# Performance work log

Hardware: AMD Instinct MI355X
Metric: run time of the kernel (lower is better)

## Reference

```python
import jax, jax.numpy as jnp
import numpy as np

N, L, S, D = 8, 1024, 4096, 512
EPS = 1e-5

def layernorm(x, g, b):
    mu = jnp.mean(x, axis=-1, keepdims=True)
    var = jnp.var(x, axis=-1, keepdims=True)
    return (x - mu) * jax.lax.rsqrt(var + EPS) * g + b

def setup_inputs() -> dict:
    key = jax.random.key(0)
    ks = jax.random.split(key, 8)
    w = lambda k, shp: jax.random.normal(k, shp, dtype=jnp.float32) * 0.02
    return {
        "x": jax.random.normal(ks[0], (N, L, D), dtype=jnp.float32),
        "source": jax.random.normal(ks[1], (N, S, D), dtype=jnp.float32),
        "Wq": w(ks[2], (D, D)),
        "Wk": w(ks[3], (D, D)),
        "Wv": w(ks[4], (D, D)),
        "Wm": w(ks[5], (D, D)),
        "W1": w(ks[6], (2 * D, 2 * D)),
        "W2": w(ks[7], (2 * D, D)),
        "g1": jnp.ones((D,), jnp.float32),
        "b1": jnp.zeros((D,), jnp.float32),
        "g2": jnp.ones((D,), jnp.float32),
        "b2": jnp.zeros((D,), jnp.float32),
    }

def reference(x, source, Wq, Wk, Wv, Wm, W1, W2, g1, b1, g2, b2):
    # projections
    q = x @ Wq          # [N, L, D]
    k = source @ Wk     # [N, S, D]
    v = source @ Wv     # [N, S, D]
    # pairwise L2 distance via ||q||^2 + ||k||^2 - 2 q.k (avoids [N,L,S,D] tensor)
    q2 = jnp.sum(q * q, axis=-1)                      # [N, L]
    k2 = jnp.sum(k * k, axis=-1)                      # [N, S]
    qk = jnp.einsum('nlc,nsc->nls', q, k)             # [N, L, S]
    dist = jnp.sqrt(jnp.maximum(q2[:, :, None] + k2[:, None, :] - 2.0 * qk, 0.0))
    attn = jax.nn.softmax(dist, axis=2)               # softmax over S (note: +distance, as in source)
    message = jnp.einsum('nls,nsc->nlc', attn, v)     # [N, L, D]
    message = layernorm(message @ Wm, g1, b1)
    h = jnp.concatenate([x, message], axis=2)         # [N, L, 2D]
    message = jax.nn.relu(h @ W1) @ W2                # [N, L, D]
    message = layernorm(message, g2, b2)
    return x + message
```

## Files before the change

kernel.cpp:

```cpp
#include <hip/hip_runtime.h>
#include <stdint.h>

typedef unsigned short u16;
typedef __attribute__((ext_vector_type(8))) short bf16x8;
typedef __attribute__((ext_vector_type(4))) float f32x4;
typedef __attribute__((ext_vector_type(4))) unsigned int u32x4;

__device__ __forceinline__ u16 f2b(float f) {
  uint32_t u = __float_as_uint(f);
  u += 0x7fffu + ((u >> 16) & 1u);
  return (u16)(u >> 16);
}
__device__ __forceinline__ float b2f(u16 h) {
  return __uint_as_float(((uint32_t)h) << 16);
}
__device__ __forceinline__ uint32_t pack2bf(float a, float b) {
#if __has_builtin(__builtin_amdgcn_cvt_pk_bf16_f32)
  typedef __attribute__((ext_vector_type(2))) __bf16 bf16x2_t;
  bf16x2_t r = __builtin_amdgcn_cvt_pk_bf16_f32(a, b);
  return __builtin_bit_cast(uint32_t, r);
#else
  return (uint32_t)f2b(a) | ((uint32_t)f2b(b) << 16);
#endif
}
__device__ __forceinline__ float fast_sqrtf(float x) {
#if __has_builtin(__builtin_amdgcn_sqrtf)
  return __builtin_amdgcn_sqrtf(x);
#else
  return sqrtf(x);
#endif
}

__device__ __forceinline__ void gload_lds16(const u16* g, u16* l) {
  __builtin_amdgcn_global_load_lds(
      (const __attribute__((address_space(1))) void*)g,
      (__attribute__((address_space(3))) void*)l, 16, 0, 0);
}

enum { EPI_BF16_T = 0, EPI_BF16_T_SQ = 1, EPI_F32_T = 2, EPI_RELU_BF16_T = 3,
       EPI_EXP_T = 4 };

template <int EPI, bool BYFAST = false>
__device__ __forceinline__ void gemm_body(
    u16* smem, const u16* A, size_t sA, int lda,
    const u16* B, size_t sB, int ldb,
    void* C, size_t sC, int ldc, int K, size_t pStride,
    const float* e_col2, const float* e_row2, float* e_l,
    int lin, int gx, int gy) {
  u16* As = smem;
  u16* Bs = smem + 8192;
  const int t = threadIdx.x;
  const int batch = lin & 7;
  const int rest = lin >> 3;
  int bx, by, part;
  if (BYFAST) {
    by = rest % gy;
    const int rx = rest / gy;
    bx = rx % gx;
    part = rx / gx;
  } else {
    bx = rest % gx;
    const int ry = rest / gx;
    by = ry % gy;
    part = ry / gy;
  }
  const int m0 = by * 128, n0 = bx * 128;
  const int koff = part * K;
  const u16* Ab = A + (size_t)batch * sA + (size_t)m0 * lda + koff;
  const u16* Bb = B + (size_t)batch * sB + (size_t)n0 * ldb + koff;
  const int srow = t >> 3;
  const int skey = (srow & 3) | (((srow >> 3) & 1) << 2);
  const int scol = ((t & 7) ^ skey) << 3;
  const u16* aS = Ab + (size_t)srow * lda + scol;
  const u16* bS = Bb + (size_t)srow * ldb + scol;
  const size_t a32 = (size_t)32 * lda, b32 = (size_t)32 * ldb;
  u16* asDst = As + t * 8;
  u16* bsDst = Bs + t * 8;

  const int w = t >> 6, lane = t & 63;
  const int wm = (w >> 1) << 6, wn = (w & 1) << 6;
  const int qd = lane >> 4, l16 = lane & 15;
  const int rbase = ((l16 >> 2) << 3) + (l16 & 3);
  const int keyA = (l16 & 3) | (((l16 >> 2) & 1) << 2);
  const int keyB = (l16 & 3) | (((l16 >> 3) & 1) << 2);
  const u16* aRow0 = As + (wm + rbase) * 64;
  const u16* bRow0 = Bs + (wn + l16) * 64;

  f32x4 acc[4][4];
#pragma unroll
  for (int i = 0; i < 4; i++)
#pragma unroll
    for (int j = 0; j < 4; j++) acc[i][j] = (f32x4)0.0f;

  for (int k0 = 0; k0 < K; k0 += 64) {
    gload_lds16(aS, asDst);
    gload_lds16(aS + a32, asDst + 2048);
    gload_lds16(aS + 2 * a32, asDst + 4096);
    gload_lds16(aS + 3 * a32, asDst + 6144);
    gload_lds16(bS, bsDst);
    gload_lds16(bS + b32, bsDst + 2048);
    gload_lds16(bS + 2 * b32, bsDst + 4096);
    gload_lds16(bS + 3 * b32, bsDst + 6144);
    aS += 64;
    bS += 64;
    __syncthreads();
#pragma unroll
    for (int s = 0; s < 2; s++) {
      const int ca = (((qd | (s << 2)) ^ keyA) << 3);
      const int cb = (((qd | (s << 2)) ^ keyB) << 3);
      bf16x8 af[4], bfr[4];
      af[0] = *(const bf16x8*)(aRow0 + ca);
      af[1] = *(const bf16x8*)(aRow0 + 4 * 64 + ca);
      af[2] = *(const bf16x8*)(aRow0 + 32 * 64 + ca);
      af[3] = *(const bf16x8*)(aRow0 + 36 * 64 + ca);
#pragma unroll
      for (int i = 0; i < 4; i++)
        bfr[i] = *(const bf16x8*)(bRow0 + i * 16 * 64 + cb);
#pragma unroll
      for (int mi = 0; mi < 4; mi++)
#pragma unroll
        for (int ni = 0; ni < 4; ni++)
          acc[mi][ni] = __builtin_amdgcn_mfma_f32_16x16x32_bf16(
              af[mi], bfr[ni], acc[mi][ni], 0, 0, 0);
    }
    __syncthreads();
  }

  const size_t cbase = (size_t)part * pStride + (size_t)batch * sC;
  const int ncols = (int)(sC / ldc);

  if constexpr (EPI == EPI_EXP_T) {
    const int nrows = (int)(sA / lda);
    const float* col2 = e_col2 + (size_t)batch * ncols;
    const float* row2 = e_row2 + (size_t)batch * nrows;
    float* lb = e_l + (size_t)batch * ncols;
    float c2v[4];
#pragma unroll
    for (int ni = 0; ni < 4; ni++) c2v[ni] = col2[n0 + wn + ni * 16 + l16];
    float cs[4] = {0.f, 0.f, 0.f, 0.f};
#pragma unroll
    for (int p = 0; p < 2; p++) {
      const int prow = m0 + wm + p * 32 + qd * 8;
      float r2v[8];
#pragma unroll
      for (int r8 = 0; r8 < 8; r8++) r2v[r8] = row2[prow + r8];
#pragma unroll
      for (int ni = 0; ni < 4; ni++) {
        const int col = n0 + wn + ni * 16 + l16;
        float pv[8];
#pragma unroll
        for (int r = 0; r < 4; r++) {
          pv[r] = __expf(fast_sqrtf(
              fmaxf(c2v[ni] + r2v[r] - 2.0f * acc[2 * p][ni][r], 0.0f)));
          pv[4 + r] = __expf(fast_sqrtf(
              fmaxf(c2v[ni] + r2v[4 + r] - 2.0f * acc[2 * p + 1][ni][r], 0.0f)));
        }
#pragma unroll
        for (int j = 0; j < 8; j++) cs[ni] += pv[j];
        u32x4 wv;
        wv[0] = pack2bf(pv[0], pv[1]);
        wv[1] = pack2bf(pv[2], pv[3]);
        wv[2] = pack2bf(pv[4], pv[5]);
        wv[3] = pack2bf(pv[6], pv[7]);
        *(u32x4*)((u16*)C + cbase + (size_t)col * ldc + prow) = wv;
      }
    }
#pragma unroll
    for (int ni = 0; ni < 4; ni++) {
      cs[ni] += __shfl_xor(cs[ni], 16);
      cs[ni] += __shfl_xor(cs[ni], 32);
    }
    if (qd == 0) {
#pragma unroll
      for (int ni = 0; ni < 4; ni++)
        atomicAdd(lb + n0 + wn + ni * 16 + l16, cs[ni]);
    }
  } else if constexpr (EPI == EPI_F32_T) {
#pragma unroll
    for (int p = 0; p < 2; p++) {
      const int prow = m0 + wm + p * 32 + qd * 8;
#pragma unroll
      for (int ni = 0; ni < 4; ni++) {
        const int col = n0 + wn + ni * 16 + l16;
        float* dst = (float*)C + cbase + (size_t)col * ldc + prow;
        *(f32x4*)dst = acc[2 * p][ni];
        *(f32x4*)(dst + 4) = acc[2 * p + 1][ni];
      }
    }
  } else {
    float cs[4] = {0.f, 0.f, 0.f, 0.f};
#pragma unroll
    for (int p = 0; p < 2; p++) {
      const int prow = m0 + wm + p * 32 + qd * 8;
#pragma unroll
      for (int ni = 0; ni < 4; ni++) {
        const int col = n0 + wn + ni * 16 + l16;
        float v[8];
#pragma unroll
        for (int r = 0; r < 4; r++) {
          v[r] = acc[2 * p][ni][r];
          v[4 + r] = acc[2 * p + 1][ni][r];
        }
        if (EPI == EPI_RELU_BF16_T) {
#pragma unroll
          for (int j = 0; j < 8; j++) v[j] = fmaxf(v[j], 0.0f);
        }
        if (EPI == EPI_BF16_T_SQ) {
#pragma unroll
          for (int j = 0; j < 8; j++) cs[ni] += v[j] * v[j];
        }
        u32x4 wv;
        wv[0] = pack2bf(v[0], v[1]);
        wv[1] = pack2bf(v[2], v[3]);
        wv[2] = pack2bf(v[4], v[5]);
        wv[3] = pack2bf(v[6], v[7]);
        *(u32x4*)((u16*)C + cbase + (size_t)col * ldc + prow) = wv;
      }
    }
    if (EPI == EPI_BF16_T_SQ) {
#pragma unroll
      for (int ni = 0; ni < 4; ni++) {
        cs[ni] += __shfl_xor(cs[ni], 16);
        cs[ni] += __shfl_xor(cs[ni], 32);
      }
      if (qd == 0) {
#pragma unroll
        for (int ni = 0; ni < 4; ni++)
          atomicAdd(e_l + (size_t)batch * ncols + n0 + wn + ni * 16 + l16,
                    cs[ni]);
      }
    }
  }
}

template <int EPI>
__global__ __launch_bounds__(256, 2) void gemm_nt(
    const u16* __restrict__ A, size_t sA, int lda,
    const u16* __restrict__ B, size_t sB, int ldb,
    void* __restrict__ C, size_t sC, int ldc, int K, size_t pStride,
    const float* __restrict__ e_col2, const float* __restrict__ e_row2,
    float* __restrict__ e_l) {
  __shared__ __align__(16) u16 smem[16384];
  const int lin = blockIdx.x + gridDim.x * (blockIdx.y + gridDim.y * blockIdx.z);
  gemm_body<EPI>(smem, A, sA, lda, B, sB, ldb, C, sC, ldc, K, pStride,
                 e_col2, e_row2, e_l, lin, gridDim.x, gridDim.y);
}

__global__ __launch_bounds__(256, 2) void proj_fused(
    const u16* __restrict__ WqT, const u16* __restrict__ WkT,
    const u16* __restrict__ WvT, const u16* __restrict__ h,
    const u16* __restrict__ sb, u16* __restrict__ q, u16* __restrict__ kb,
    u16* __restrict__ vT, float* __restrict__ q2, float* __restrict__ k2) {
  __shared__ __align__(16) u16 smem[16384];
  const int lin = blockIdx.x;
  if (lin < 256) {
    gemm_body<EPI_BF16_T_SQ, true>(smem, WqT, 0, 512, h, (size_t)1024 * 1024,
                                   1024, q, (size_t)1024 * 512, 512, 512, 0,
                                   nullptr, nullptr, q2, lin, 8, 4);
  } else if (lin < 1280) {
    gemm_body<EPI_BF16_T_SQ, true>(smem, WkT, 0, 512, sb, (size_t)4096 * 512,
                                   512, kb, (size_t)4096 * 512, 512, 512, 0,
                                   nullptr, nullptr, k2, lin - 256, 32, 4);
  } else {
    gemm_body<EPI_BF16_T>(smem, sb, (size_t)4096 * 512, 512, WvT, 0, 512,
                          vT, (size_t)512 * 4096, 4096, 512, 0, nullptr,
                          nullptr, nullptr, lin - 1280, 4, 32);
  }
}

__global__ __launch_bounds__(256) void prep_all(
    const float* __restrict__ x, const float* __restrict__ sc,
    u16* __restrict__ h, u16* __restrict__ sb, float* __restrict__ q2,
    float* __restrict__ k2, float* __restrict__ lsum,
    const float* __restrict__ Wq, const float* __restrict__ Wk,
    const float* __restrict__ Wv, const float* __restrict__ Wm,
    const float* __restrict__ W1, const float* __restrict__ W2,
    u16* __restrict__ WqT, u16* __restrict__ WkT, u16* __restrict__ WvT,
    u16* __restrict__ WmT2, u16* __restrict__ W1T, u16* __restrict__ W2T) {
  __shared__ float tile[32][33];
  const int blk = blockIdx.x;
  if (blk < 20528) {
    const size_t i = (size_t)blk * 256 + threadIdx.x;
    if (i < 1048576) {
      const float4 f = ((const float4*)x)[i];
      const int e = (int)(i << 2);
      const int row = e >> 9, col = e & 511;
      *(ushort4*)(h + ((size_t)row << 10) + col) =
          make_ushort4(f2b(f.x), f2b(f.y), f2b(f.z), f2b(f.w));
    } else if (i < 5242880) {
      const size_t j = i - 1048576;
      const float4 f = ((const float4*)sc)[j];
      *(ushort4*)(sb + (j << 2)) =
          make_ushort4(f2b(f.x), f2b(f.y), f2b(f.z), f2b(f.w));
    } else {
      const size_t j = i - 5242880;
      const float4 z = {0.f, 0.f, 0.f, 0.f};
      if (j < 2048) ((float4*)q2)[j] = z;
      else if (j < 10240) ((float4*)k2)[j - 2048] = z;
      else ((float4*)lsum)[j - 10240] = z;
    }
    return;
  }
  const int tb = blk - 20528;
  const float* W;
  u16* WT;
  int R, Cn, ldT, dup = 0, c0, r0;
  if (tb < 1024) {
    const int z = tb >> 8, local = tb & 255;
    switch (z) {
      case 0: W = Wq; WT = WqT; break;
      case 1: W = Wk; WT = WkT; break;
      case 2: W = Wv; WT = WvT; break;
      default: W = Wm; WT = WmT2; dup = 1; break;
    }
    R = 512; Cn = 512; ldT = dup ? 1024 : 512;
    c0 = (local & 15) << 5; r0 = (local >> 4) << 5;
  } else if (tb < 2048) {
    const int local = tb - 1024;
    W = W1; WT = W1T; R = 1024; Cn = 1024; ldT = 1024;
    c0 = (local & 31) << 5; r0 = (local >> 5) << 5;
  } else {
    const int local = tb - 2048;
    W = W2; WT = W2T; R = 1024; Cn = 512; ldT = 1024;
    c0 = (local & 15) << 5; r0 = (local >> 4) << 5;
  }
  const int tx = threadIdx.x & 31, ty = threadIdx.x >> 5;
  for (int i = ty; i < 32; i += 8)
    tile[i][tx] = W[(size_t)(r0 + i) * Cn + c0 + tx];
  __syncthreads();
  for (int i = ty; i < 32; i += 8) {
    const u16 v = f2b(tile[tx][i]);
    WT[(size_t)(c0 + i) * ldT + r0 + tx] = v;
    if (dup) WT[(size_t)(c0 + i) * ldT + 512 + r0 + tx] = v;
  }
}

__global__ __launch_bounds__(128) void ln_to_h(const float* __restrict__ mm,
                                               const float* __restrict__ lsum,
                                               const float* __restrict__ g,
                                               const float* __restrict__ b,
                                               u16* __restrict__ h) {
  const size_t row = blockIdx.x;
  const int t = threadIdx.x;
  const float inv = 1.0f / lsum[row];
  const float4 fa = ((const float4*)(mm + row * 512))[t];
  const float4 fb = ((const float4*)(mm + 4194304 + row * 512))[t];
  float4 f;
  f.x = (fa.x + fb.x) * inv; f.y = (fa.y + fb.y) * inv;
  f.z = (fa.z + fb.z) * inv; f.w = (fa.w + fb.w) * inv;
  float s = f.x + f.y + f.z + f.w;
  float sq = f.x * f.x + f.y * f.y + f.z * f.z + f.w * f.w;
#pragma unroll
  for (int off = 32; off; off >>= 1) { s += __shfl_xor(s, off); sq += __shfl_xor(sq, off); }
  __shared__ float rs_[2], rq_[2];
  if ((t & 63) == 0) { rs_[t >> 6] = s; rq_[t >> 6] = sq; }
  __syncthreads();
  s = rs_[0] + rs_[1]; sq = rq_[0] + rq_[1];
  const float mu = s * (1.0f / 512.0f);
  const float rstd = rsqrtf(sq * (1.0f / 512.0f) - mu * mu + 1e-5f);
  const float4 gv = ((const float4*)g)[t], bv = ((const float4*)b)[t];
  ushort4 o = make_ushort4(f2b((f.x - mu) * rstd * gv.x + bv.x),
                           f2b((f.y - mu) * rstd * gv.y + bv.y),
                           f2b((f.z - mu) * rstd * gv.z + bv.z),
                           f2b((f.w - mu) * rstd * gv.w + bv.w));
  *(ushort4*)(h + (row << 10) + 512 + (t << 2)) = o;
}

__global__ __launch_bounds__(128) void ln_residual(const float* __restrict__ m2,
                                                   const float* __restrict__ x,
                                                   const float* __restrict__ g,
                                                   const float* __restrict__ b,
                                                   float* __restrict__ out) {
  const size_t row = blockIdx.x;
  const int t = threadIdx.x;
  const float4 fa = ((const float4*)(m2 + row * 512))[t];
  const float4 fb = ((const float4*)(m2 + 4194304 + row * 512))[t];
  float4 f;
  f.x = fa.x + fb.x; f.y = fa.y + fb.y; f.z = fa.z + fb.z; f.w = fa.w + fb.w;
  float s = f.x + f.y + f.z + f.w;
  float sq = f.x * f.x + f.y * f.y + f.z * f.z + f.w * f.w;
#pragma unroll
  for (int off = 32; off; off >>= 1) { s += __shfl_xor(s, off); sq += __shfl_xor(sq, off); }
  __shared__ float rs_[2], rq_[2];
  if ((t & 63) == 0) { rs_[t >> 6] = s; rq_[t >> 6] = sq; }
  __syncthreads();
  s = rs_[0] + rs_[1]; sq = rq_[0] + rq_[1];
  const float mu = s * (1.0f / 512.0f);
  const float rstd = rsqrtf(sq * (1.0f / 512.0f) - mu * mu + 1e-5f);
  const float4 gv = ((const float4*)g)[t], bv = ((const float4*)b)[t];
  const float4 xv = ((const float4*)(x + row * 512))[t];
  float4 o;
  o.x = xv.x + (f.x - mu) * rstd * gv.x + bv.x;
  o.y = xv.y + (f.y - mu) * rstd * gv.y + bv.y;
  o.z = xv.z + (f.z - mu) * rstd * gv.z + bv.z;
  o.w = xv.w + (f.w - mu) * rstd * gv.w + bv.w;
  ((float4*)(out + row * 512))[t] = o;
}

extern "C" void kernel_launch(void* const* d_in, const int* in_sizes, int n_in,
                              void* d_out, int out_size, void* d_ws, size_t ws_size,
                              hipStream_t stream) {
  const float* x  = (const float*)d_in[0];
  const float* sc = (const float*)d_in[1];
  const float* Wq = (const float*)d_in[2];
  const float* Wk = (const float*)d_in[3];
  const float* Wv = (const float*)d_in[4];
  const float* Wm = (const float*)d_in[5];
  const float* W1 = (const float*)d_in[6];
  const float* W2 = (const float*)d_in[7];
  const float* g1 = (const float*)d_in[8];
  const float* b1 = (const float*)d_in[9];
  const float* g2 = (const float*)d_in[10];
  const float* b2 = (const float*)d_in[11];
  float* out = (float*)d_out;
  char* ws = (char*)d_ws;

  constexpr int N = 8, L = 1024, S = 4096, D = 512;
  u16*   h    = (u16*)(ws + 0);
  u16*   sb   = (u16*)(ws + 16777216);
  u16*   WqT  = (u16*)(ws + 50331648);
  u16*   WkT  = (u16*)(ws + 50855936);
  u16*   WvT  = (u16*)(ws + 51380224);
  u16*   WmT2 = (u16*)(ws + 51904512);
  u16*   W1T  = (u16*)(ws + 52953088);
  u16*   W2T  = (u16*)(ws + 55050240);
  u16*   q    = (u16*)(ws + 56098816);
  u16*   kb   = (u16*)(ws + 64487424);
  u16*   vT   = (u16*)(ws + 98041856);
  float* lsum = (float*)(ws + 131596288);
  float* q2   = (float*)(ws + 131629056);
  float* k2   = (float*)(ws + 131661824);
  u16*   qk   = (u16*)(ws + 164790272);
  u16*   msg2 = (u16*)(ws + 56098816);
  float* mm   = (float*)(ws + 72876032);
  u16*   hh   = (u16*)(ws + 72876032);
  float* m2   = (float*)(ws + 98041856);

  prep_all<<<dim3(23088), 256, 0, stream>>>(x, sc, h, sb, q2, k2, lsum,
                                            Wq, Wk, Wv, Wm, W1, W2,
                                            WqT, WkT, WvT, WmT2, W1T, W2T);

  proj_fused<<<dim3(2304), 256, 0, stream>>>(WqT, WkT, WvT, h, sb, q, kb, vT,
                                             q2, k2);

  gemm_nt<EPI_EXP_T><<<dim3(8, 32, 8), 256, 0, stream>>>(
      kb, (size_t)S * 512, 512, q, (size_t)L * 512, 512, qk, (size_t)L * S, S,
      512, 0, q2, k2, lsum);
  gemm_nt<EPI_BF16_T><<<dim3(8, 4, 16), 256, 0, stream>>>(
      vT, (size_t)D * S, S, qk, (size_t)L * S, S, msg2, (size_t)L * 1024, 1024,
      2048, 512, nullptr, nullptr, nullptr);

  gemm_nt<EPI_F32_T><<<dim3(8, 4, 16), 256, 0, stream>>>(
      WmT2, 0, 1024, msg2, (size_t)L * 1024, 1024, mm, (size_t)L * 512, 512,
      512, (size_t)(N * L) * 512, nullptr, nullptr, nullptr);
  ln_to_h<<<dim3(N * L), 128, 0, stream>>>(mm, lsum, g1, b1, h);

  gemm_nt<EPI_RELU_BF16_T><<<dim3(8, 8, 8), 256, 0, stream>>>(
      W1T, 0, 1024, h, (size_t)L * 1024, 1024, hh, (size_t)L * 1024, 1024, 1024,
      0, nullptr, nullptr, nullptr);
  gemm_nt<EPI_F32_T><<<dim3(8, 4, 16), 256, 0, stream>>>(
      W2T, 0, 1024, hh, (size_t)L * 1024, 1024, m2, (size_t)L * 512, 512, 512,
      (size_t)(N * L) * 512, nullptr, nullptr, nullptr);

  ln_residual<<<dim3(N * L), 128, 0, stream>>>(m2, x, g2, b2, out);
}
```

Measured before the change: 352.9 us.

## Fold Wm into Wv to eliminate the separate message projection GEMM

Precomputes Wv·Wm as one 512x512 weight with a small GEMM, then uses it in the value projection so that attn@V directly yields message@Wm. This removes the bf16 intermediate message buffer and the Wm GEMM over all N*L rows, writing the split-K f32 partials straight into mm for the layernorm. It adds a tiny weight GEMM launch and one extra bf16 rounding of the combined weight.

```diff
diff --git a/kernel.cpp b/kernel.cpp
--- a/kernel.cpp
+++ b/kernel.cpp
@@ -246,9 +246,18 @@
                  e_col2, e_row2, e_l, lin, gridDim.x, gridDim.y);
 }
 
+template <int EPI>
+__global__ __launch_bounds__(256, 2) void gemm_nt_nb(
+    const u16* __restrict__ A, int lda, const u16* __restrict__ B, int ldb,
+    void* __restrict__ C, size_t sC, int ldc, int K, int gx, int gy) {
+  __shared__ __align__(16) u16 smem[16384];
+  gemm_body<EPI>(smem, A, 0, lda, B, 0, ldb, C, sC, ldc, K, 0,
+                 nullptr, nullptr, nullptr, (int)(blockIdx.x << 3), gx, gy);
+}
+
 __global__ __launch_bounds__(256, 2) void proj_fused(
     const u16* __restrict__ WqT, const u16* __restrict__ WkT,
-    const u16* __restrict__ WvT, const u16* __restrict__ h,
+    const u16* __restrict__ WvmT, const u16* __restrict__ h,
     const u16* __restrict__ sb, u16* __restrict__ q, u16* __restrict__ kb,
     u16* __restrict__ vT, float* __restrict__ q2, float* __restrict__ k2) {
   __shared__ __align__(16) u16 smem[16384];
@@ -262,7 +271,7 @@
                                    512, kb, (size_t)4096 * 512, 512, 512, 0,
                                    nullptr, nullptr, k2, lin - 256, 32, 4);
   } else {
-    gemm_body<EPI_BF16_T>(smem, sb, (size_t)4096 * 512, 512, WvT, 0, 512,
+    gemm_body<EPI_BF16_T>(smem, sb, (size_t)4096 * 512, 512, WvmT, 0, 512,
                           vT, (size_t)512 * 4096, 4096, 512, 0, nullptr,
                           nullptr, nullptr, lin - 1280, 4, 32);
   }
@@ -275,8 +284,8 @@
     const float* __restrict__ Wq, const float* __restrict__ Wk,
     const float* __restrict__ Wv, const float* __restrict__ Wm,
     const float* __restrict__ W1, const float* __restrict__ W2,
-    u16* __restrict__ WqT, u16* __restrict__ WkT, u16* __restrict__ WvT,
-    u16* __restrict__ WmT2, u16* __restrict__ W1T, u16* __restrict__ W2T) {
+    u16* __restrict__ WqT, u16* __restrict__ WkT, u16* __restrict__ WvN,
+    u16* __restrict__ WmT, u16* __restrict__ W1T, u16* __restrict__ W2T) {
   __shared__ float tile[32][33];
   const int blk = blockIdx.x;
   if (blk < 20528) {
@@ -304,16 +313,16 @@
   const int tb = blk - 20528;
   const float* W;
   u16* WT;
-  int R, Cn, ldT, dup = 0, c0, r0;
+  int R, Cn, ldT, c0, r0, notr = 0;
   if (tb < 1024) {
     const int z = tb >> 8, local = tb & 255;
     switch (z) {
       case 0: W = Wq; WT = WqT; break;
       case 1: W = Wk; WT = WkT; break;
-      case 2: W = Wv; WT = WvT; break;
-      default: W = Wm; WT = WmT2; dup = 1; break;
-    }
-    R = 512; Cn = 512; ldT = dup ? 1024 : 512;
+      case 2: W = Wv; WT = WvN; notr = 1; break;
+      default: W = Wm; WT = WmT; break;
+    }
+    R = 512; Cn = 512; ldT = 512;
     c0 = (local & 15) << 5; r0 = (local >> 4) << 5;
   } else if (tb < 2048) {
     const int local = tb - 1024;
@@ -328,10 +337,12 @@
   for (int i = ty; i < 32; i += 8)
     tile[i][tx] = W[(size_t)(r0 + i) * Cn + c0 + tx];
   __syncthreads();
-  for (int i = ty; i < 32; i += 8) {
-    const u16 v = f2b(tile[tx][i]);
-    WT[(size_t)(c0 + i) * ldT + r0 + tx] = v;
-    if (dup) WT[(size_t)(c0 + i) * ldT + 512 + r0 + tx] = v;
+  if (notr) {
+    for (int i = ty; i < 32; i += 8)
+      WT[(size_t)(r0 + i) * Cn + c0 + tx] = f2b(tile[i][tx]);
+  } else {
+    for (int i = ty; i < 32; i += 8)
+      WT[(size_t)(c0 + i) * ldT + r0 + tx] = f2b(tile[tx][i]);
   }
 }
 
@@ -420,8 +431,8 @@
   u16*   sb   = (u16*)(ws + 16777216);
   u16*   WqT  = (u16*)(ws + 50331648);
   u16*   WkT  = (u16*)(ws + 50855936);
-  u16*   WvT  = (u16*)(ws + 51380224);
-  u16*   WmT2 = (u16*)(ws + 51904512);
+  u16*   WvN  = (u16*)(ws + 51380224);
+  u16*   WmT  = (u16*)(ws + 51904512);
   u16*   W1T  = (u16*)(ws + 52953088);
   u16*   W2T  = (u16*)(ws + 55050240);
   u16*   q    = (u16*)(ws + 56098816);
@@ -431,28 +442,28 @@
   float* q2   = (float*)(ws + 131629056);
   float* k2   = (float*)(ws + 131661824);
   u16*   qk   = (u16*)(ws + 164790272);
-  u16*   msg2 = (u16*)(ws + 56098816);
-  float* mm   = (float*)(ws + 72876032);
-  u16*   hh   = (u16*)(ws + 72876032);
+  u16*   WvmT = (u16*)(ws + 164790272);
+  float* mm   = (float*)(ws + 64487424);
+  u16*   hh   = (u16*)(ws + 64487424);
   float* m2   = (float*)(ws + 98041856);
 
   prep_all<<<dim3(23088), 256, 0, stream>>>(x, sc, h, sb, q2, k2, lsum,
                                             Wq, Wk, Wv, Wm, W1, W2,
-                                            WqT, WkT, WvT, WmT2, W1T, W2T);
-
-  proj_fused<<<dim3(2304), 256, 0, stream>>>(WqT, WkT, WvT, h, sb, q, kb, vT,
+                                            WqT, WkT, WvN, WmT, W1T, W2T);
+
+  gemm_nt_nb<EPI_BF16_T><<<dim3(16), 256, 0, stream>>>(
+      WvN, 512, WmT, 512, WvmT, (size_t)512 * 512, 512, 512, 4, 4);
+
+  proj_fused<<<dim3(2304), 256, 0, stream>>>(WqT, WkT, WvmT, h, sb, q, kb, vT,
                                              q2, k2);
 
   gemm_nt<EPI_EXP_T><<<dim3(8, 32, 8), 256, 0, stream>>>(
       kb, (size_t)S * 512, 512, q, (size_t)L * 512, 512, qk, (size_t)L * S, S,
       512, 0, q2, k2, lsum);
-  gemm_nt<EPI_BF16_T><<<dim3(8, 4, 16), 256, 0, stream>>>(
-      vT, (size_t)D * S, S, qk, (size_t)L * S, S, msg2, (size_t)L * 1024, 1024,
-      2048, 512, nullptr, nullptr, nullptr);
-
   gemm_nt<EPI_F32_T><<<dim3(8, 4, 16), 256, 0, stream>>>(
-      WmT2, 0, 1024, msg2, (size_t)L * 1024, 1024, mm, (size_t)L * 512, 512,
-      512, (size_t)(N * L) * 512, nullptr, nullptr, nullptr);
+      vT, (size_t)D * S, S, qk, (size_t)L * S, S, mm, (size_t)L * 512, 512,
+      2048, (size_t)(N * L) * 512, nullptr, nullptr, nullptr);
+
   ln_to_h<<<dim3(N * L), 128, 0, stream>>>(mm, lsum, g1, b1, h);
 
   gemm_nt<EPI_RELU_BF16_T><<<dim3(8, 8, 8), 256, 0, stream>>>(
```

New measurement: 362.9 us. 2.8% more time.
